# Kernel optimization log

Measured on AMD Instinct MI355X. Metric: run time of the kernel, lower is better.

Reference implementation:

```python
import jax, jax.numpy as jnp
import numpy as np

B, T, F, D, HD = 16, 512, 16, 256, 256


def _init(k, shape, fan_in):
    return (jax.random.uniform(k, shape, minval=-1.0, maxval=1.0) / np.sqrt(fan_in)).astype(jnp.float32)


def setup_inputs() -> dict:
    key = jax.random.key(0)
    ks = jax.random.split(key, 16)
    return {
        "x": jax.random.normal(ks[0], (B, T, F), dtype=jnp.float32),
        # per-variable encoder params, batched over F (Linear(1,D) + GRN(D,HD,D))
        "w1": _init(ks[1], (F, D), 1), "b1": _init(ks[2], (F, D), 1),
        "fc1_w": _init(ks[3], (F, D, HD), D), "fc1_b": _init(ks[4], (F, HD), D),
        "fc2_w": _init(ks[5], (F, HD, D), HD), "fc2_b": _init(ks[6], (F, D), HD),
        "glu_w": _init(ks[7], (F, D, 2 * D), D), "glu_b": _init(ks[8], (F, 2 * D), D),
        "ln_g": jnp.ones((F, D), jnp.float32), "ln_b": jnp.zeros((F, D), jnp.float32),
        # weight GRN(F, HD, F); skip is Identity since d_in == d_out
        "wg_fc1_w": _init(ks[9], (F, HD), F), "wg_fc1_b": _init(ks[10], (HD,), F),
        "wg_fc2_w": _init(ks[11], (HD, F), HD), "wg_fc2_b": _init(ks[12], (F,), HD),
        "wg_glu_w": _init(ks[13], (F, 2 * F), F), "wg_glu_b": _init(ks[14], (2 * F,), F),
        "wg_ln_g": jnp.ones((F,), jnp.float32), "wg_ln_b": jnp.zeros((F,), jnp.float32),
    }


def _layernorm(x, g, b, eps=1e-5):
    m = jnp.mean(x, axis=-1, keepdims=True)
    v = jnp.var(x, axis=-1, keepdims=True)
    return (x - m) * jax.lax.rsqrt(v + eps) * g + b


def reference(x, w1, b1, fc1_w, fc1_b, fc2_w, fc2_b, glu_w, glu_b, ln_g, ln_b,
              wg_fc1_w, wg_fc1_b, wg_fc2_w, wg_fc2_b, wg_glu_w, wg_glu_b,
              wg_ln_g, wg_ln_b):
    # --- per-variable towers, batched over F (dropout is identity at eval) ---
    h0 = jax.nn.relu(x[..., None] * w1 + b1)                       # [B,T,F,D]
    y = jax.nn.elu(jnp.einsum('btfd,fdh->btfh', h0, fc1_w) + fc1_b)
    y = jnp.einsum('btfh,fhd->btfd', y, fc2_w) + fc2_b
    g = jnp.einsum('btfd,fde->btfe', y, glu_w) + glu_b             # [B,T,F,2D]
    a, gate = jnp.split(g, 2, axis=-1)
    H = _layernorm(h0 + a * jax.nn.sigmoid(gate), ln_g, ln_b)      # [B,T,F,D]
    # --- variable-weight GRN (time_distributed=True) ---
    yw = jax.nn.elu(x @ wg_fc1_w + wg_fc1_b)
    yw = yw @ wg_fc2_w + wg_fc2_b
    gw = x @ jnp.zeros((F, 0), x.dtype) if False else yw @ wg_glu_w + wg_glu_b
    aw, gatew = jnp.split(gw, 2, axis=-1)
    w = _layernorm(x + aw * jax.nn.sigmoid(gatew), wg_ln_g, wg_ln_b)
    w = jax.nn.softmax(w, axis=-1)                                 # [B,T,F]
    z = jnp.einsum('btfd,btf->btd', H, w)                          # [B,T,D]
    return z, w
```

## Files before the change

### kernel.cpp

```cpp
#include <hip/hip_runtime.h>
#include <hip/hip_bf16.h>

#define NBT 8192
#define NF  16
#define ND  256
#define NH  256
#define N2D 512

typedef short bf16x8 __attribute__((ext_vector_type(8)));
typedef float f32x4 __attribute__((ext_vector_type(4)));
typedef unsigned short u16x8 __attribute__((ext_vector_type(8)));

__device__ __forceinline__ float bf2f(unsigned short u) {
  return __uint_as_float(((unsigned)u) << 16);
}
__device__ __forceinline__ unsigned short f2bf(float f) {
  unsigned u = __float_as_uint(f);
  return (unsigned short)((u + 0x7FFFu + ((u >> 16) & 1u)) >> 16);
}

#define GLOAD16(src, dst)                                                     \
  __builtin_amdgcn_global_load_lds(                                           \
      (const __attribute__((address_space(1))) unsigned int*)(src),           \
      (__attribute__((address_space(3))) unsigned int*)(dst), 16, 0, 0)

__global__ __launch_bounds__(256) void wgrn_kernel(
    const float* __restrict__ x, const float* __restrict__ fw1,
    const float* __restrict__ fb1, const float* __restrict__ fw2,
    const float* __restrict__ fb2, const float* __restrict__ gwt,
    const float* __restrict__ gbt, const float* __restrict__ lng,
    const float* __restrict__ lnb, float* __restrict__ wout) {
  __shared__ float w1t[256 * 16];
  __shared__ float w2s[256 * 16];
  const int tid = threadIdx.x;
  for (int i = tid; i < 4096; i += 256) {
    int ff = i >> 8, j = i & 255;
    w1t[j * 16 + ff] = fw1[i];
    w2s[i] = fw2[i];
  }
  __syncthreads();
  const int sub  = tid & 7;
  const int rowi = tid >> 3;
  const int bt   = blockIdx.x * 32 + rowi;
  float xr[16];
#pragma unroll
  for (int i = 0; i < 4; ++i)
    *(float4*)&xr[i * 4] = *(const float4*)(x + (size_t)bt * 16 + i * 4);
  float acc2[16];
#pragma unroll
  for (int q = 0; q < 16; ++q) acc2[q] = 0.f;
  for (int j = sub; j < 256; j += 8) {
    float h = fb1[j];
    const float* wr = &w1t[j * 16];
#pragma unroll
    for (int q = 0; q < 16; ++q) h = fmaf(xr[q], wr[q], h);
    h = h > 0.f ? h : expm1f(h);
    const float* w2r = &w2s[j * 16];
#pragma unroll
    for (int q = 0; q < 16; ++q) acc2[q] = fmaf(h, w2r[q], acc2[q]);
  }
#pragma unroll
  for (int off = 1; off < 8; off <<= 1) {
#pragma unroll
    for (int q = 0; q < 16; ++q) acc2[q] += __shfl_xor(acc2[q], off);
  }
#pragma unroll
  for (int q = 0; q < 16; ++q) acc2[q] += fb2[q];
  float gw[32];
#pragma unroll
  for (int k = 0; k < 32; ++k) {
    float s = gbt[k];
#pragma unroll
    for (int q = 0; q < 16; ++q) s = fmaf(acc2[q], gwt[q * 32 + k], s);
    gw[k] = s;
  }
  float v[16];
  float mean = 0.f;
#pragma unroll
  for (int q = 0; q < 16; ++q) {
    float sg = 1.f / (1.f + __expf(-gw[16 + q]));
    v[q] = fmaf(gw[q], sg, xr[q]);
    mean += v[q];
  }
  mean *= (1.f / 16.f);
  float var = 0.f;
#pragma unroll
  for (int q = 0; q < 16; ++q) { float d = v[q] - mean; var = fmaf(d, d, var); }
  var *= (1.f / 16.f);
  float rstd = rsqrtf(var + 1e-5f);
  float mx = -1e30f;
#pragma unroll
  for (int q = 0; q < 16; ++q) {
    v[q] = (v[q] - mean) * rstd * lng[q] + lnb[q];
    mx = fmaxf(mx, v[q]);
  }
  float se = 0.f;
#pragma unroll
  for (int q = 0; q < 16; ++q) { v[q] = __expf(v[q] - mx); se += v[q]; }
  float inv = 1.f / se;
  if (sub == 0) {
#pragma unroll
    for (int i = 0; i < 4; ++i) {
      float4 o = { v[i*4+0]*inv, v[i*4+1]*inv, v[i*4+2]*inv, v[i*4+3]*inv };
      *(float4*)(wout + (size_t)bt * 16 + i * 4) = o;
    }
  }
}

__global__ void transpose_all(const float* __restrict__ fc1_w,
                              const float* __restrict__ fc2_w,
                              const float* __restrict__ glu_w,
                              unsigned short* __restrict__ fc1t,
                              unsigned short* __restrict__ fc2t,
                              unsigned short* __restrict__ glut) {
  __shared__ float tile[32][33];
  const int which = blockIdx.z >> 4;
  const int f     = blockIdx.z & 15;
  const float* src;
  unsigned short* dst;
  int K, N, bx = blockIdx.x;
  if (which == 0)      { src = fc1_w; dst = fc1t; K = ND; N = NH; }
  else if (which == 1) { src = fc2_w; dst = fc2t; K = NH; N = ND; }
  else                 { src = glu_w; dst = glut; K = ND; N = N2D;
                         bx += (which == 3) ? 8 : 0; }
  if (bx * 32 >= N) return;
  const float* s = src + (size_t)f * K * N;
  unsigned short* d = dst + (size_t)f * K * N;
  const int k0 = blockIdx.y * 32, n0 = bx * 32;
  const int tx = threadIdx.x, ty = threadIdx.y;
#pragma unroll
  for (int i = 0; i < 32; i += 8)
    tile[ty + i][tx] = s[(size_t)(k0 + ty + i) * N + n0 + tx];
  __syncthreads();
#pragma unroll
  for (int i = 0; i < 32; i += 8)
    d[(size_t)(n0 + ty + i) * K + k0 + tx] = f2bf(tile[tx][ty + i]);
}

__global__ __launch_bounds__(256, 4) void g1_kernel(
    const float* __restrict__ x, const float* __restrict__ w1,
    const float* __restrict__ b1, const unsigned short* __restrict__ fc1t,
    const float* __restrict__ fc1_b, unsigned short* __restrict__ y1) {
  __shared__ __align__(16) char arena[34816];
  __shared__ float xw[128];
  unsigned short* abuf = (unsigned short*)arena;
  unsigned short* bbuf = (unsigned short*)(arena + 17408);
  unsigned short* cbuf = (unsigned short*)arena;
  const int tid = threadIdx.x, lane = tid & 63, wid = tid >> 6;
  const int rl = lane & 15, kc = lane >> 4;
  int hb = blockIdx.x + 2 * (blockIdx.y + 64 * blockIdx.z);
  int L  = (hb & 7) * 256 + (hb >> 3);
  const int f = L >> 7, m0 = ((L >> 1) & 63) * 128, n0 = (L & 1) * 128;
  const unsigned short* Bf = fc1t + (size_t)f * NH * ND;
  const float* w1f = w1 + f * ND;
  const float* b1f = b1 + f * ND;
  if (tid < 128) xw[tid] = x[(size_t)(m0 + tid) * NF + f];
  const int wm = (wid >> 1) * 64, wn = (wid & 1) * 64;

  f32x4 acc[4][4];
#pragma unroll
  for (int m = 0; m < 4; ++m)
#pragma unroll
    for (int n = 0; n < 4; ++n) acc[m][n] = (f32x4){0.f, 0.f, 0.f, 0.f};

  for (int kt = 0; kt < ND; kt += 64) {
    __syncthreads();
#pragma unroll
    for (int i = 0; i < 4; ++i) {
      int s = tid + 256 * i;
      int row = s >> 3, sl = s & 7;
      const unsigned short* gb =
          Bf + (size_t)(n0 + row) * ND + kt + ((sl ^ (row & 7)) << 3);
      GLOAD16(gb, (char*)bbuf + (wid * 64 + 256 * i) * 16);
    }
#pragma unroll
    for (int i = 0; i < 4; ++i) {
      int vi = tid + 256 * i;
      int row = vi >> 3, c8 = vi & 7, c = kt + c8 * 8;
      float xv = xw[row];
      float4 wa = *(const float4*)(w1f + c);
      float4 wb = *(const float4*)(w1f + c + 4);
      float4 ba = *(const float4*)(b1f + c);
      float4 bb = *(const float4*)(b1f + c + 4);
      u16x8 o;
      o[0] = f2bf(fmaxf(fmaf(xv, wa.x, ba.x), 0.f));
      o[1] = f2bf(fmaxf(fmaf(xv, wa.y, ba.y), 0.f));
      o[2] = f2bf(fmaxf(fmaf(xv, wa.z, ba.z), 0.f));
      o[3] = f2bf(fmaxf(fmaf(xv, wa.w, ba.w), 0.f));
      o[4] = f2bf(fmaxf(fmaf(xv, wb.x, bb.x), 0.f));
      o[5] = f2bf(fmaxf(fmaf(xv, wb.y, bb.y), 0.f));
      o[6] = f2bf(fmaxf(fmaf(xv, wb.z, bb.z), 0.f));
      o[7] = f2bf(fmaxf(fmaf(xv, wb.w, bb.w), 0.f));
      *(u16x8*)(abuf + row * 68 + c8 * 8) = o;
    }
    __syncthreads();
#pragma unroll
    for (int kk = 0; kk < 2; ++kk) {
      bf16x8 av[4], bv[4];
      int s = kk * 4 + kc;
#pragma unroll
      for (int m = 0; m < 4; ++m) {
        int r = wm + m * 16 + rl;
        av[m] = *(const bf16x8*)(abuf + r * 68 + s * 8);
      }
#pragma unroll
      for (int n = 0; n < 4; ++n) {
        int rr = wn + n * 16 + rl;
        int ps = s ^ (rr & 7);
        bv[n] = *(const bf16x8*)((const char*)bbuf + rr * 128 + ps * 16);
      }
#pragma unroll
      for (int m = 0; m < 4; ++m)
#pragma unroll
        for (int n = 0; n < 4; ++n)
          acc[m][n] = __builtin_amdgcn_mfma_f32_16x16x32_bf16(av[m], bv[n],
                                                              acc[m][n], 0, 0, 0);
    }
  }

  __syncthreads();
  const int rq = lane >> 4;
#pragma unroll
  for (int n = 0; n < 4; ++n) {
    int cl = wn + n * 16 + rl;
    float bvv = fc1_b[f * NH + n0 + cl];
#pragma unroll
    for (int m = 0; m < 4; ++m) {
#pragma unroll
      for (int j = 0; j < 4; ++j) {
        int r = wm + m * 16 + rq * 4 + j;
        float v = acc[m][n][j] + bvv;
        v = v > 0.f ? v : expm1f(v);
        cbuf[r * 136 + cl] = f2bf(v);
      }
    }
  }
  __syncthreads();
#pragma unroll
  for (int v = 0; v < 8; ++v) {
    int row = (tid >> 4) + v * 16, chunk = tid & 15;
    u16x8 val = *(const u16x8*)(cbuf + row * 136 + chunk * 8);
    *(u16x8*)(y1 + ((size_t)f * NBT + m0 + row) * NH + n0 + chunk * 8) = val;
  }
}

__global__ __launch_bounds__(512, 4) void g2_kernel(
    const unsigned short* __restrict__ y1,
    const unsigned short* __restrict__ fc2t, const float* __restrict__ fc2_b,
    unsigned short* __restrict__ y2) {
  __shared__ __align__(16) char arena[49152];
  unsigned short* abuf = (unsigned short*)arena;
  unsigned short* bbuf = (unsigned short*)(arena + 16384);
  unsigned short* cbuf = (unsigned short*)arena;
  const int tid = threadIdx.x, lane = tid & 63, wid = tid >> 6;
  const int rl = lane & 15, kc = lane >> 4;
  int hb = blockIdx.x + 64 * blockIdx.y;
  int L  = (hb & 7) * 128 + (hb >> 3);
  const int f = L >> 6, m0 = (L & 63) * 128;
  const unsigned short* Af = y1 + (size_t)f * NBT * NH;
  const unsigned short* Bf = fc2t + (size_t)f * ND * NH;
  const int wm = (wid >> 2) * 64, wn = (wid & 3) * 64;

  f32x4 acc[4][4];
#pragma unroll
  for (int m = 0; m < 4; ++m)
#pragma unroll
    for (int n = 0; n < 4; ++n) acc[m][n] = (f32x4){0.f, 0.f, 0.f, 0.f};

  for (int kt = 0; kt < NH; kt += 64) {
    __syncthreads();
#pragma unroll
    for (int i = 0; i < 2; ++i) {
      int s = tid + 512 * i;
      int row = s >> 3, sl = s & 7;
      const unsigned short* ga =
          Af + (size_t)(m0 + row) * NH + kt + ((sl ^ (row & 7)) << 3);
      GLOAD16(ga, (char*)abuf + (wid * 64 + 512 * i) * 16);
    }
#pragma unroll
    for (int i = 0; i < 4; ++i) {
      int s = tid + 512 * i;
      int row = s >> 3, sl = s & 7;
      const unsigned short* gb =
          Bf + (size_t)row * NH + kt + ((sl ^ (row & 7)) << 3);
      GLOAD16(gb, (char*)bbuf + (wid * 64 + 512 * i) * 16);
    }
    __syncthreads();
#pragma unroll
    for (int kk = 0; kk < 2; ++kk) {
      bf16x8 av[4], bv[4];
      int s = kk * 4 + kc;
#pragma unroll
      for (int m = 0; m < 4; ++m) {
        int r = wm + m * 16 + rl;
        int ps = s ^ (r & 7);
        av[m] = *(const bf16x8*)((const char*)abuf + r * 128 + ps * 16);
      }
#pragma unroll
      for (int n = 0; n < 4; ++n) {
        int rr = wn + n * 16 + rl;
        int ps = s ^ (rr & 7);
        bv[n] = *(const bf16x8*)((const char*)bbuf + rr * 128 + ps * 16);
      }
#pragma unroll
      for (int m = 0; m < 4; ++m)
#pragma unroll
        for (int n = 0; n < 4; ++n)
          acc[m][n] = __builtin_amdgcn_mfma_f32_16x16x32_bf16(av[m], bv[n],
                                                              acc[m][n], 0, 0, 0);
    }
  }

  __syncthreads();
  const int rq = lane >> 4;
  const int hsel = (wid & 3) >> 1;
#pragma unroll
  for (int h = 0; h < 2; ++h) {
    if (h) __syncthreads();
    if (hsel == h) {
#pragma unroll
      for (int n = 0; n < 4; ++n) {
        int c = wn + n * 16 + rl;
        int cl = c - h * 128;
        float bvv = fc2_b[f * ND + c];
#pragma unroll
        for (int m = 0; m < 4; ++m) {
#pragma unroll
          for (int j = 0; j < 4; ++j) {
            int r = wm + m * 16 + rq * 4 + j;
            cbuf[r * 136 + cl] = f2bf(acc[m][n][j] + bvv);
          }
        }
      }
    }
    __syncthreads();
#pragma unroll
    for (int v = 0; v < 4; ++v) {
      int row = (tid >> 4) + v * 32, chunk = tid & 15;
      u16x8 val = *(const u16x8*)(cbuf + row * 136 + chunk * 8);
      *(u16x8*)(y2 + ((size_t)f * NBT + m0 + row) * ND + h * 128 + chunk * 8) =
          val;
    }
  }
}

__global__ __launch_bounds__(512, 4) void g3_kernel(
    const unsigned short* __restrict__ y2,
    const unsigned short* __restrict__ glut, const float* __restrict__ glu_b,
    const float* __restrict__ x, const float* __restrict__ w1,
    const float* __restrict__ b1, const float* __restrict__ ln_g,
    const float* __restrict__ ln_b, unsigned short* __restrict__ H) {
  __shared__ __align__(16) char arena[73728];
  __shared__ float xw[64];
  __shared__ float2 sums[8][64];
  __shared__ float2 sums2[64];
  unsigned short* abuf = (unsigned short*)arena;
  unsigned short* bbuf = (unsigned short*)(arena + 8192);
  unsigned short* vbuf = (unsigned short*)arena;

  const int tid = threadIdx.x, lane = tid & 63, wid = tid >> 6;
  const int rl = lane & 15, rq = lane >> 4;
  int hb = blockIdx.x + 128 * blockIdx.y;
  int L  = (hb & 7) * 256 + (hb >> 3);
  const int f = L >> 7, m0 = (L & 127) * 64;
  const unsigned short* Af = y2 + (size_t)f * NBT * ND;
  const unsigned short* Bf = glut + (size_t)f * ND * N2D;
  const float* w1f = w1 + f * ND;
  const float* b1f = b1 + f * ND;
  const int colb = wid * 32;
  if (tid < 64) xw[tid] = x[(size_t)(m0 + tid) * NF + f];

  f32x4 acc[4][4];
#pragma unroll
  for (int m = 0; m < 4; ++m)
#pragma unroll
    for (int n = 0; n < 4; ++n) acc[m][n] = (f32x4){0.f, 0.f, 0.f, 0.f};

  for (int kt = 0; kt < ND; kt += 64) {
    __syncthreads();
    {
      int s = tid;
      int row = s >> 3, sl = s & 7;
      const unsigned short* ga =
          Af + (size_t)(m0 + row) * ND + kt + ((sl ^ (row & 7)) << 3);
      GLOAD16(ga, (char*)abuf + (wid * 64) * 16);
    }
#pragma unroll
    for (int i = 0; i < 8; ++i) {
      int s = tid + 512 * i;
      int row = s >> 3, sl = s & 7;
      const unsigned short* gb =
          Bf + (size_t)row * ND + kt + ((sl ^ (row & 7)) << 3);
      GLOAD16(gb, (char*)bbuf + (wid * 64 + 512 * i) * 16);
    }
    __syncthreads();
#pragma unroll
    for (int kk = 0; kk < 2; ++kk) {
      bf16x8 av[4], bv[4];
      int s = kk * 4 + rq;
#pragma unroll
      for (int m = 0; m < 4; ++m) {
        int r = m * 16 + rl;
        int ps = s ^ (r & 7);
        av[m] = *(const bf16x8*)((const char*)abuf + r * 128 + ps * 16);
      }
#pragma unroll
      for (int n = 0; n < 4; ++n) {
        int rr = (n < 2) ? (colb + n * 16 + rl)
                         : (256 + colb + (n - 2) * 16 + rl);
        int ps = s ^ (rr & 7);
        bv[n] = *(const bf16x8*)((const char*)bbuf + rr * 128 + ps * 16);
      }
#pragma unroll
      for (int m = 0; m < 4; ++m)
#pragma unroll
        for (int n = 0; n < 4; ++n)
          acc[m][n] = __builtin_amdgcn_mfma_f32_16x16x32_bf16(av[m], bv[n],
                                                              acc[m][n], 0, 0, 0);
    }
  }

#pragma unroll
  for (int n = 0; n < 2; ++n) {
    int cA = colb + n * 16 + rl;
    float ab_ = glu_b[f * N2D + cA];
    float gb_ = glu_b[f * N2D + 256 + cA];
    float w1c = w1f[cA], b1c = b1f[cA];
#pragma unroll
    for (int m = 0; m < 4; ++m) {
#pragma unroll
      for (int j = 0; j < 4; ++j) {
        int r = m * 16 + rq * 4 + j;
        float a = acc[m][n][j] + ab_;
        float g = acc[m][n + 2][j] + gb_;
        float sg = 1.f / (1.f + __expf(-g));
        float h0 = fmaxf(fmaf(xw[r], w1c, b1c), 0.f);
        acc[m][n][j] = fmaf(a, sg, h0);
      }
    }
  }
#pragma unroll
  for (int m = 0; m < 4; ++m) {
#pragma unroll
    for (int j = 0; j < 4; ++j) {
      float s = acc[m][0][j] + acc[m][1][j];
      float q = fmaf(acc[m][0][j], acc[m][0][j],
                     acc[m][1][j] * acc[m][1][j]);
#pragma unroll
      for (int off = 1; off < 16; off <<= 1) {
        s += __shfl_xor(s, off);
        q += __shfl_xor(q, off);
      }
      if (rl == 0) sums[wid][m * 16 + rq * 4 + j] = make_float2(s, q);
    }
  }
  __syncthreads();
  if (tid < 64) {
    float tot = 0.f, tot2 = 0.f;
#pragma unroll
    for (int wv = 0; wv < 8; ++wv) {
      float2 p = sums[wv][tid];
      tot += p.x;
      tot2 += p.y;
    }
    float mean = tot * (1.f / 256.f);
    float var  = tot2 * (1.f / 256.f) - mean * mean;
    sums2[tid] = make_float2(mean, rsqrtf(var + 1e-5f));
  }
  __syncthreads();
#pragma unroll
  for (int n = 0; n < 2; ++n) {
    int cA = colb + n * 16 + rl;
    float lg = ln_g[f * ND + cA], lb = ln_b[f * ND + cA];
#pragma unroll
    for (int m = 0; m < 4; ++m) {
#pragma unroll
      for (int j = 0; j < 4; ++j) {
        int r = m * 16 + rq * 4 + j;
        float2 mr = sums2[r];
        vbuf[r * 264 + cA] = f2bf(fmaf((acc[m][n][j] - mr.x) * mr.y, lg, lb));
      }
    }
  }
  __syncthreads();
  {
    int row = tid >> 3, chunk = tid & 7;
    unsigned short* Hrow = H + ((size_t)f * NBT + m0 + row) * ND;
#pragma unroll
    for (int v = 0; v < 4; ++v) {
      u16x8 val = *(const u16x8*)(vbuf + row * 264 + chunk * 8 + v * 64);
      *(u16x8*)(Hrow + chunk * 8 + v * 64) = val;
    }
  }
}

__global__ __launch_bounds__(256) void combine_kernel(
    const unsigned short* __restrict__ H, const float* __restrict__ w,
    float* __restrict__ z) {
  int idx = blockIdx.x * 256 + threadIdx.x;
  int bt = idx >> 5;
  int d  = (idx & 31) << 3;
  float a[8];
#pragma unroll
  for (int j = 0; j < 8; ++j) a[j] = 0.f;
#pragma unroll
  for (int f = 0; f < 16; ++f) {
    u16x8 hv = *(const u16x8*)(H + ((size_t)f * NBT + bt) * ND + d);
    float wvv = w[bt * 16 + f];
#pragma unroll
    for (int j = 0; j < 8; ++j) a[j] = fmaf(bf2f(hv[j]), wvv, a[j]);
  }
  float4 o0 = {a[0], a[1], a[2], a[3]};
  float4 o1 = {a[4], a[5], a[6], a[7]};
  *(float4*)(z + (size_t)bt * ND + d)     = o0;
  *(float4*)(z + (size_t)bt * ND + d + 4) = o1;
}

extern "C" void kernel_launch(void* const* d_in, const int* in_sizes, int n_in,
                              void* d_out, int out_size, void* d_ws,
                              size_t ws_size, hipStream_t stream) {
  const float* x        = (const float*)d_in[0];
  const float* w1       = (const float*)d_in[1];
  const float* b1       = (const float*)d_in[2];
  const float* fc1_w    = (const float*)d_in[3];
  const float* fc1_b    = (const float*)d_in[4];
  const float* fc2_w    = (const float*)d_in[5];
  const float* fc2_b    = (const float*)d_in[6];
  const float* glu_w    = (const float*)d_in[7];
  const float* glu_b    = (const float*)d_in[8];
  const float* ln_g     = (const float*)d_in[9];
  const float* ln_b     = (const float*)d_in[10];
  const float* wg_fc1_w = (const float*)d_in[11];
  const float* wg_fc1_b = (const float*)d_in[12];
  const float* wg_fc2_w = (const float*)d_in[13];
  const float* wg_fc2_b = (const float*)d_in[14];
  const float* wg_glu_w = (const float*)d_in[15];
  const float* wg_glu_b = (const float*)d_in[16];
  const float* wg_ln_g  = (const float*)d_in[17];
  const float* wg_ln_b  = (const float*)d_in[18];

  char* ws = (char*)d_ws;
  unsigned short* fc1t = (unsigned short*)ws;
  unsigned short* fc2t = fc1t + (size_t)NF * NH * ND;
  unsigned short* glut = fc2t + (size_t)NF * ND * NH;
  unsigned short* y1   = (unsigned short*)(ws + (8ull << 20));
  unsigned short* y2   = (unsigned short*)(ws + (72ull << 20));
  unsigned short* Hbuf = (unsigned short*)(ws + (136ull << 20));

  float* zout = (float*)d_out;
  float* wout = zout + (size_t)NBT * ND;

  wgrn_kernel<<<256, 256, 0, stream>>>(x, wg_fc1_w, wg_fc1_b, wg_fc2_w,
                                       wg_fc2_b, wg_glu_w, wg_glu_b, wg_ln_g,
                                       wg_ln_b, wout);
  transpose_all<<<dim3(16, 8, 64), dim3(32, 8), 0, stream>>>(
      fc1_w, fc2_w, glu_w, fc1t, fc2t, glut);

  g1_kernel<<<dim3(NH / 128, NBT / 128, NF), 256, 0, stream>>>(
      x, w1, b1, fc1t, fc1_b, y1);
  g2_kernel<<<dim3(NBT / 128, NF), 512, 0, stream>>>(y1, fc2t, fc2_b, y2);
  g3_kernel<<<dim3(NBT / 64, NF), 512, 0, stream>>>(y2, glut, glu_b, x, w1, b1,
                                                    ln_g, ln_b, Hbuf);
  combine_kernel<<<(NBT * ND / 8) / 256, 256, 0, stream>>>(Hbuf, wout, zout);

  (void)in_sizes; (void)n_in; (void)out_size; (void)ws_size;
}
```

Baseline: 227.0 us.

## Load GEMM weight fragments directly from global memory instead of staging in LDS

In all three GEMM kernels, the B-operand (weight) tiles are no longer staged into shared memory via global_load_lds. Each wave now reads its MFMA B fragments straight from global memory into registers, and the LDS arenas shrink to match. This removes LDS staging traffic and shared-memory footprint, which could raise occupancy. In exchange, weight reads become per-wave global loads with no sharing across waves, so they depend on cache hits and add global latency inside the inner loop.

After: 250.2 us. +10.2%, slower.

```diff
diff --git a/kernel.cpp b/kernel.cpp
--- a/kernel.cpp
+++ b/kernel.cpp
@@ -144,7 +144,6 @@
   __shared__ __align__(16) char arena[34816];
   __shared__ float xw[128];
   unsigned short* abuf = (unsigned short*)arena;
-  unsigned short* bbuf = (unsigned short*)(arena + 17408);
   unsigned short* cbuf = (unsigned short*)arena;
   const int tid = threadIdx.x, lane = tid & 63, wid = tid >> 6;
   const int rl = lane & 15, kc = lane >> 4;
@@ -165,14 +164,6 @@
 
   for (int kt = 0; kt < ND; kt += 64) {
     __syncthreads();
-#pragma unroll
-    for (int i = 0; i < 4; ++i) {
-      int s = tid + 256 * i;
-      int row = s >> 3, sl = s & 7;
-      const unsigned short* gb =
-          Bf + (size_t)(n0 + row) * ND + kt + ((sl ^ (row & 7)) << 3);
-      GLOAD16(gb, (char*)bbuf + (wid * 64 + 256 * i) * 16);
-    }
 #pragma unroll
     for (int i = 0; i < 4; ++i) {
       int vi = tid + 256 * i;
@@ -199,15 +190,15 @@
       bf16x8 av[4], bv[4];
       int s = kk * 4 + kc;
 #pragma unroll
+      for (int n = 0; n < 4; ++n) {
+        int rr = wn + n * 16 + rl;
+        bv[n] = *(const bf16x8*)(Bf + (size_t)(n0 + rr) * ND + kt + kk * 32 +
+                                 kc * 8);
+      }
+#pragma unroll
       for (int m = 0; m < 4; ++m) {
         int r = wm + m * 16 + rl;
         av[m] = *(const bf16x8*)(abuf + r * 68 + s * 8);
-      }
-#pragma unroll
-      for (int n = 0; n < 4; ++n) {
-        int rr = wn + n * 16 + rl;
-        int ps = s ^ (rr & 7);
-        bv[n] = *(const bf16x8*)((const char*)bbuf + rr * 128 + ps * 16);
       }
 #pragma unroll
       for (int m = 0; m < 4; ++m)
@@ -248,9 +239,8 @@
     const unsigned short* __restrict__ y1,
     const unsigned short* __restrict__ fc2t, const float* __restrict__ fc2_b,
     unsigned short* __restrict__ y2) {
-  __shared__ __align__(16) char arena[49152];
+  __shared__ __align__(16) char arena[34816];
   unsigned short* abuf = (unsigned short*)arena;
-  unsigned short* bbuf = (unsigned short*)(arena + 16384);
   unsigned short* cbuf = (unsigned short*)arena;
   const int tid = threadIdx.x, lane = tid & 63, wid = tid >> 6;
   const int rl = lane & 15, kc = lane >> 4;
@@ -277,30 +267,21 @@
           Af + (size_t)(m0 + row) * NH + kt + ((sl ^ (row & 7)) << 3);
       GLOAD16(ga, (char*)abuf + (wid * 64 + 512 * i) * 16);
     }
-#pragma unroll
-    for (int i = 0; i < 4; ++i) {
-      int s = tid + 512 * i;
-      int row = s >> 3, sl = s & 7;
-      const unsigned short* gb =
-          Bf + (size_t)row * NH + kt + ((sl ^ (row & 7)) << 3);
-      GLOAD16(gb, (char*)bbuf + (wid * 64 + 512 * i) * 16);
-    }
     __syncthreads();
 #pragma unroll
     for (int kk = 0; kk < 2; ++kk) {
       bf16x8 av[4], bv[4];
       int s = kk * 4 + kc;
+#pragma unroll
+      for (int n = 0; n < 4; ++n) {
+        int rr = wn + n * 16 + rl;
+        bv[n] = *(const bf16x8*)(Bf + (size_t)rr * NH + kt + kk * 32 + kc * 8);
+      }
 #pragma unroll
       for (int m = 0; m < 4; ++m) {
         int r = wm + m * 16 + rl;
         int ps = s ^ (r & 7);
         av[m] = *(const bf16x8*)((const char*)abuf + r * 128 + ps * 16);
-      }
-#pragma unroll
-      for (int n = 0; n < 4; ++n) {
-        int rr = wn + n * 16 + rl;
-        int ps = s ^ (rr & 7);
-        bv[n] = *(const bf16x8*)((const char*)bbuf + rr * 128 + ps * 16);
       }
 #pragma unroll
       for (int m = 0; m < 4; ++m)
@@ -350,12 +331,11 @@
     const float* __restrict__ x, const float* __restrict__ w1,
     const float* __restrict__ b1, const float* __restrict__ ln_g,
     const float* __restrict__ ln_b, unsigned short* __restrict__ H) {
-  __shared__ __align__(16) char arena[73728];
+  __shared__ __align__(16) char arena[33792];
   __shared__ float xw[64];
   __shared__ float2 sums[8][64];
   __shared__ float2 sums2[64];
   unsigned short* abuf = (unsigned short*)arena;
-  unsigned short* bbuf = (unsigned short*)(arena + 8192);
   unsigned short* vbuf = (unsigned short*)arena;
 
   const int tid = threadIdx.x, lane = tid & 63, wid = tid >> 6;
@@ -385,31 +365,23 @@
           Af + (size_t)(m0 + row) * ND + kt + ((sl ^ (row & 7)) << 3);
       GLOAD16(ga, (char*)abuf + (wid * 64) * 16);
     }
-#pragma unroll
-    for (int i = 0; i < 8; ++i) {
-      int s = tid + 512 * i;
-      int row = s >> 3, sl = s & 7;
-      const unsigned short* gb =
-          Bf + (size_t)row * ND + kt + ((sl ^ (row & 7)) << 3);
-      GLOAD16(gb, (char*)bbuf + (wid * 64 + 512 * i) * 16);
-    }
     __syncthreads();
 #pragma unroll
     for (int kk = 0; kk < 2; ++kk) {
       bf16x8 av[4], bv[4];
       int s = kk * 4 + rq;
+#pragma unroll
+      for (int n = 0; n < 4; ++n) {
+        int brow = (n < 2) ? (colb + n * 16 + rl)
+                           : (256 + colb + (n - 2) * 16 + rl);
+        bv[n] = *(const bf16x8*)(Bf + (size_t)brow * ND + kt + kk * 32 +
+                                 rq * 8);
+      }
 #pragma unroll
       for (int m = 0; m < 4; ++m) {
         int r = m * 16 + rl;
         int ps = s ^ (r & 7);
         av[m] = *(const bf16x8*)((const char*)abuf + r * 128 + ps * 16);
-      }
-#pragma unroll
-      for (int n = 0; n < 4; ++n) {
-        int rr = (n < 2) ? (colb + n * 16 + rl)
-                         : (256 + colb + (n - 2) * 16 + rl);
-        int ps = s ^ (rr & 7);
-        bv[n] = *(const bf16x8*)((const char*)bbuf + rr * 128 + ps * 16);
       }
 #pragma unroll
       for (int m = 0; m < 4; ++m)
```

## Stage full A tile in LDS once and stream GLU weights from global into registers

Applied to the files above, without the earlier changes.

The GLU GEMM kernel now loads the entire 64x256 activation tile into LDS with one swizzled async copy. The per-k-step LDS staging of the B (weight) tile is gone; each lane reads its B fragments directly from global memory into registers, double-buffered. This removes the repeated barriers per k-tile and shrinks the LDS arena, which may raise occupancy. In exchange each wave issues more global loads for weights, relying on cache hits across blocks that share the same feature. The launch dims are rewritten as literal constants with the same values.

Result: slower. 254.4 us (+12.1%).

```diff
diff --git a/kernel.cpp b/kernel.cpp
--- a/kernel.cpp
+++ b/kernel.cpp
@@ -350,12 +350,11 @@
     const float* __restrict__ x, const float* __restrict__ w1,
     const float* __restrict__ b1, const float* __restrict__ ln_g,
     const float* __restrict__ ln_b, unsigned short* __restrict__ H) {
-  __shared__ __align__(16) char arena[73728];
+  __shared__ __align__(16) char arena[33792];
   __shared__ float xw[64];
   __shared__ float2 sums[8][64];
   __shared__ float2 sums2[64];
-  unsigned short* abuf = (unsigned short*)arena;
-  unsigned short* bbuf = (unsigned short*)(arena + 8192);
+  unsigned short* Abuf = (unsigned short*)arena;
   unsigned short* vbuf = (unsigned short*)arena;
 
   const int tid = threadIdx.x, lane = tid & 63, wid = tid >> 6;
@@ -370,52 +369,74 @@
   const int colb = wid * 32;
   if (tid < 64) xw[tid] = x[(size_t)(m0 + tid) * NF + f];
 
+#pragma unroll
+  for (int i = 0; i < 4; ++i) {
+    int g = tid + 512 * i;
+    int row = g >> 5, s = g & 31;
+    int srcs = (s & 24) | ((s ^ row) & 7);
+    GLOAD16(Af + (size_t)(m0 + row) * ND + srcs * 8, (char*)Abuf + g * 16);
+  }
+
+  const unsigned short* bp[4];
+#pragma unroll
+  for (int n = 0; n < 4; ++n) {
+    int brow = (n < 2) ? (colb + n * 16 + rl) : (256 + colb + (n - 2) * 16 + rl);
+    bp[n] = Bf + (size_t)brow * ND + rq * 8;
+  }
+
   f32x4 acc[4][4];
 #pragma unroll
   for (int m = 0; m < 4; ++m)
 #pragma unroll
     for (int n = 0; n < 4; ++n) acc[m][n] = (f32x4){0.f, 0.f, 0.f, 0.f};
 
-  for (int kt = 0; kt < ND; kt += 64) {
-    __syncthreads();
+  __syncthreads();
+
+  bf16x8 b0[4], b1v[4];
+#pragma unroll
+  for (int n = 0; n < 4; ++n) b0[n] = *(const bf16x8*)(bp[n]);
+
+#pragma unroll
+  for (int tt = 0; tt < 4; ++tt) {
+    const int t0 = 2 * tt, t1 = 2 * tt + 1;
+#pragma unroll
+    for (int n = 0; n < 4; ++n)
+      b1v[n] = *(const bf16x8*)(bp[n] + t1 * 32);
     {
-      int s = tid;
-      int row = s >> 3, sl = s & 7;
-      const unsigned short* ga =
-          Af + (size_t)(m0 + row) * ND + kt + ((sl ^ (row & 7)) << 3);
-      GLOAD16(ga, (char*)abuf + (wid * 64) * 16);
-    }
-#pragma unroll
-    for (int i = 0; i < 8; ++i) {
-      int s = tid + 512 * i;
-      int row = s >> 3, sl = s & 7;
-      const unsigned short* gb =
-          Bf + (size_t)row * ND + kt + ((sl ^ (row & 7)) << 3);
-      GLOAD16(gb, (char*)bbuf + (wid * 64 + 512 * i) * 16);
-    }
-    __syncthreads();
-#pragma unroll
-    for (int kk = 0; kk < 2; ++kk) {
-      bf16x8 av[4], bv[4];
-      int s = kk * 4 + rq;
+      bf16x8 av[4];
 #pragma unroll
       for (int m = 0; m < 4; ++m) {
-        int r = m * 16 + rl;
-        int ps = s ^ (r & 7);
-        av[m] = *(const bf16x8*)((const char*)abuf + r * 128 + ps * 16);
-      }
-#pragma unroll
-      for (int n = 0; n < 4; ++n) {
-        int rr = (n < 2) ? (colb + n * 16 + rl)
-                         : (256 + colb + (n - 2) * 16 + rl);
-        int ps = s ^ (rr & 7);
-        bv[n] = *(const bf16x8*)((const char*)bbuf + rr * 128 + ps * 16);
+        int row = m * 16 + rl;
+        int gr = t0 * 4 + rq;
+        int g2 = (gr & 24) | ((gr ^ row) & 7);
+        av[m] = *(const bf16x8*)(Abuf + row * 256 + g2 * 8);
       }
 #pragma unroll
       for (int m = 0; m < 4; ++m)
 #pragma unroll
         for (int n = 0; n < 4; ++n)
-          acc[m][n] = __builtin_amdgcn_mfma_f32_16x16x32_bf16(av[m], bv[n],
+          acc[m][n] = __builtin_amdgcn_mfma_f32_16x16x32_bf16(av[m], b0[n],
+                                                              acc[m][n], 0, 0, 0);
+    }
+    if (tt < 3) {
+#pragma unroll
+      for (int n = 0; n < 4; ++n)
+        b0[n] = *(const bf16x8*)(bp[n] + (t1 + 1) * 32);
+    }
+    {
+      bf16x8 av[4];
+#pragma unroll
+      for (int m = 0; m < 4; ++m) {
+        int row = m * 16 + rl;
+        int gr = t1 * 4 + rq;
+        int g2 = (gr & 24) | ((gr ^ row) & 7);
+        av[m] = *(const bf16x8*)(Abuf + row * 256 + g2 * 8);
+      }
+#pragma unroll
+      for (int m = 0; m < 4; ++m)
+#pragma unroll
+        for (int n = 0; n < 4; ++n)
+          acc[m][n] = __builtin_amdgcn_mfma_f32_16x16x32_bf16(av[m], b1v[n],
                                                               acc[m][n], 0, 0, 0);
     }
   }
@@ -556,11 +577,10 @@
   transpose_all<<<dim3(16, 8, 64), dim3(32, 8), 0, stream>>>(
       fc1_w, fc2_w, glu_w, fc1t, fc2t, glut);
 
-  g1_kernel<<<dim3(NH / 128, NBT / 128, NF), 256, 0, stream>>>(
-      x, w1, b1, fc1t, fc1_b, y1);
-  g2_kernel<<<dim3(NBT / 128, NF), 512, 0, stream>>>(y1, fc2t, fc2_b, y2);
-  g3_kernel<<<dim3(NBT / 64, NF), 512, 0, stream>>>(y2, glut, glu_b, x, w1, b1,
-                                                    ln_g, ln_b, Hbuf);
+  g1_kernel<<<dim3(2, 64, 16), 256, 0, stream>>>(x, w1, b1, fc1t, fc1_b, y1);
+  g2_kernel<<<dim3(64, 16), 512, 0, stream>>>(y1, fc2t, fc2_b, y2);
+  g3_kernel<<<dim3(128, 16), 512, 0, stream>>>(y2, glut, glu_b, x, w1, b1,
+                                               ln_g, ln_b, Hbuf);
   combine_kernel<<<(NBT * ND / 8) / 256, 256, 0, stream>>>(Hbuf, wout, zout);
 
   (void)in_sizes; (void)n_in; (void)out_size; (void)ws_size;
```

## Fuse softmax-weighted combine into GLU epilogue via atomic adds

Applied to the files above, without the earlier changes.

The combine step is folded into the g3 epilogue. Each block multiplies its normalized H values by the per-row softmax weight and atomically adds them into z, which a new kernel zeroes first. This removes the bf16 H buffer write/read and the separate combine kernel. In exchange it issues many fp32 atomics (16-way contention per output element), adds a zeroing pass, and makes the summation order nondeterministic.

Result: slower. 283.7 us (+24.9%).

```diff
diff --git a/kernel.cpp b/kernel.cpp
--- a/kernel.cpp
+++ b/kernel.cpp
@@ -105,6 +105,11 @@
       *(float4*)(wout + (size_t)bt * 16 + i * 4) = o;
     }
   }
+}
+
+__global__ __launch_bounds__(256) void zzero_kernel(float* __restrict__ z) {
+  size_t i = ((size_t)blockIdx.x * 256 + threadIdx.x) * 4;
+  *(float4*)(z + i) = (float4){0.f, 0.f, 0.f, 0.f};
 }
 
 __global__ void transpose_all(const float* __restrict__ fc1_w,
@@ -349,14 +354,15 @@
     const unsigned short* __restrict__ glut, const float* __restrict__ glu_b,
     const float* __restrict__ x, const float* __restrict__ w1,
     const float* __restrict__ b1, const float* __restrict__ ln_g,
-    const float* __restrict__ ln_b, unsigned short* __restrict__ H) {
+    const float* __restrict__ ln_b, const float* __restrict__ wsoft,
+    float* __restrict__ zout) {
   __shared__ __align__(16) char arena[73728];
   __shared__ float xw[64];
+  __shared__ float wwv[64];
   __shared__ float2 sums[8][64];
   __shared__ float2 sums2[64];
   unsigned short* abuf = (unsigned short*)arena;
   unsigned short* bbuf = (unsigned short*)(arena + 8192);
-  unsigned short* vbuf = (unsigned short*)arena;
 
   const int tid = threadIdx.x, lane = tid & 63, wid = tid >> 6;
   const int rl = lane & 15, rq = lane >> 4;
@@ -368,7 +374,10 @@
   const float* w1f = w1 + f * ND;
   const float* b1f = b1 + f * ND;
   const int colb = wid * 32;
-  if (tid < 64) xw[tid] = x[(size_t)(m0 + tid) * NF + f];
+  if (tid < 64) {
+    xw[tid]  = x[(size_t)(m0 + tid) * NF + f];
+    wwv[tid] = wsoft[(size_t)(m0 + tid) * NF + f];
+  }
 
   f32x4 acc[4][4];
 #pragma unroll
@@ -478,42 +487,11 @@
       for (int j = 0; j < 4; ++j) {
         int r = m * 16 + rq * 4 + j;
         float2 mr = sums2[r];
-        vbuf[r * 264 + cA] = f2bf(fmaf((acc[m][n][j] - mr.x) * mr.y, lg, lb));
-      }
-    }
-  }
-  __syncthreads();
-  {
-    int row = tid >> 3, chunk = tid & 7;
-    unsigned short* Hrow = H + ((size_t)f * NBT + m0 + row) * ND;
-#pragma unroll
-    for (int v = 0; v < 4; ++v) {
-      u16x8 val = *(const u16x8*)(vbuf + row * 264 + chunk * 8 + v * 64);
-      *(u16x8*)(Hrow + chunk * 8 + v * 64) = val;
-    }
-  }
-}
-
-__global__ __launch_bounds__(256) void combine_kernel(
-    const unsigned short* __restrict__ H, const float* __restrict__ w,
-    float* __restrict__ z) {
-  int idx = blockIdx.x * 256 + threadIdx.x;
-  int bt = idx >> 5;
-  int d  = (idx & 31) << 3;
-  float a[8];
-#pragma unroll
-  for (int j = 0; j < 8; ++j) a[j] = 0.f;
-#pragma unroll
-  for (int f = 0; f < 16; ++f) {
-    u16x8 hv = *(const u16x8*)(H + ((size_t)f * NBT + bt) * ND + d);
-    float wvv = w[bt * 16 + f];
-#pragma unroll
-    for (int j = 0; j < 8; ++j) a[j] = fmaf(bf2f(hv[j]), wvv, a[j]);
-  }
-  float4 o0 = {a[0], a[1], a[2], a[3]};
-  float4 o1 = {a[4], a[5], a[6], a[7]};
-  *(float4*)(z + (size_t)bt * ND + d)     = o0;
-  *(float4*)(z + (size_t)bt * ND + d + 4) = o1;
+        float Hv = fmaf((acc[m][n][j] - mr.x) * mr.y, lg, lb);
+        unsafeAtomicAdd(zout + (size_t)(m0 + r) * ND + cA, Hv * wwv[r]);
+      }
+    }
+  }
 }
 
 extern "C" void kernel_launch(void* const* d_in, const int* in_sizes, int n_in,
@@ -545,23 +523,21 @@
   unsigned short* glut = fc2t + (size_t)NF * ND * NH;
   unsigned short* y1   = (unsigned short*)(ws + (8ull << 20));
   unsigned short* y2   = (unsigned short*)(ws + (72ull << 20));
-  unsigned short* Hbuf = (unsigned short*)(ws + (136ull << 20));
 
   float* zout = (float*)d_out;
   float* wout = zout + (size_t)NBT * ND;
 
+  zzero_kernel<<<(NBT * ND / 4) / 256, 256, 0, stream>>>(zout);
   wgrn_kernel<<<256, 256, 0, stream>>>(x, wg_fc1_w, wg_fc1_b, wg_fc2_w,
                                        wg_fc2_b, wg_glu_w, wg_glu_b, wg_ln_g,
                                        wg_ln_b, wout);
   transpose_all<<<dim3(16, 8, 64), dim3(32, 8), 0, stream>>>(
       fc1_w, fc2_w, glu_w, fc1t, fc2t, glut);
 
-  g1_kernel<<<dim3(NH / 128, NBT / 128, NF), 256, 0, stream>>>(
-      x, w1, b1, fc1t, fc1_b, y1);
-  g2_kernel<<<dim3(NBT / 128, NF), 512, 0, stream>>>(y1, fc2t, fc2_b, y2);
-  g3_kernel<<<dim3(NBT / 64, NF), 512, 0, stream>>>(y2, glut, glu_b, x, w1, b1,
-                                                    ln_g, ln_b, Hbuf);
-  combine_kernel<<<(NBT * ND / 8) / 256, 256, 0, stream>>>(Hbuf, wout, zout);
+  g1_kernel<<<dim3(2, 64, 16), 256, 0, stream>>>(x, w1, b1, fc1t, fc1_b, y1);
+  g2_kernel<<<dim3(64, 16), 512, 0, stream>>>(y1, fc2t, fc2_b, y2);
+  g3_kernel<<<dim3(128, 16), 512, 0, stream>>>(y2, glut, glu_b, x, w1, b1,
+                                               ln_g, ln_b, wout, zout);
 
   (void)in_sizes; (void)n_in; (void)out_size; (void)ws_size;
 }
```
